# Performance work log

Hardware: AMD Instinct MI355X
Metric: run time of the kernel (lower is better)

Reference implementation:

```python
import jax, jax.numpy as jnp
import numpy as np

B, N, D, H = 1, 4096, 1024, 16
K = D // H
ROPE_BASE = 10000.0


def _rope_cos_sin(n, k, base, dtype):
    # GPT-NeoX style rotary embedding: inv_freq over even dims, emb = cat(freqs, freqs)
    inv_freq = 1.0 / (base ** (jnp.arange(0, k, 2, dtype=jnp.float32) / k))  # [K/2]
    pos = jnp.arange(n, dtype=jnp.float32)
    freqs = pos[:, None] * inv_freq[None, :]              # [N, K/2]
    emb = jnp.concatenate([freqs, freqs], axis=-1)        # [N, K]
    return jnp.cos(emb).astype(dtype), jnp.sin(emb).astype(dtype)


def _rotate_half(x):
    x1, x2 = jnp.split(x, 2, axis=-1)
    return jnp.concatenate([-x2, x1], axis=-1)


def setup_inputs() -> dict:
    key = jax.random.key(0)
    kx, kq, ko = jax.random.split(key, 3)
    x = jax.random.normal(kx, (B, N, D), dtype=jnp.float32)
    # torch Linear weights: [out_features, in_features], y = x @ W^T
    w_qkv = jax.random.normal(kq, (3 * H * K, D), dtype=jnp.float32) / np.sqrt(D)
    w_out = jax.random.normal(ko, (D, D), dtype=jnp.float32) / np.sqrt(D)
    return {"x": x, "w_qkv": w_qkv, "w_out": w_out}


def reference(x, w_qkv, w_out):
    b, n, d = x.shape
    qkv = jnp.einsum('bnd,ed->bne', x, w_qkv).reshape(b, n, 3, H, K)
    q, k, v = qkv[:, :, 0], qkv[:, :, 1], qkv[:, :, 2]   # [B, N, H, K]
    cos, sin = _rope_cos_sin(n, K, ROPE_BASE, x.dtype)    # [N, K]
    cos = cos[None, :, None, :]
    sin = sin[None, :, None, :]
    q = q * cos + _rotate_half(q) * sin
    k = k * cos + _rotate_half(k) * sin
    # explicit O(N^2) score matrix, as in the original module
    scores = jnp.einsum('bnhk,bmhk->bnhm', q, k) / np.sqrt(K).astype(x.dtype)
    causal_mask = jnp.tril(jnp.ones((n, n), dtype=bool))  # [N, M]
    scores = jnp.where(causal_mask[None, :, None, :], scores, jnp.finfo(x.dtype).min)
    probs = jax.nn.softmax(scores, axis=-1)
    attn = jnp.einsum('bnhm,bmhk->bnhk', probs, v).reshape(b, n, d)
    return jnp.einsum('bnd,ed->bne', attn, w_out)
```

## Files before the change

kernel.cpp:

```cpp
#include <hip/hip_runtime.h>
#include <hip/hip_bf16.h>
#include <math.h>

#define N_SEQ 4096
#define DIM   1024
#define NHEAD 16
#define HDIM  64
#define E3    3072

typedef short bf16x8 __attribute__((ext_vector_type(8)));
typedef float f32x4  __attribute__((ext_vector_type(4)));
typedef unsigned int u32;

#if __has_builtin(__builtin_amdgcn_exp2f)
#define EXP2(x) __builtin_amdgcn_exp2f(x)
#else
#define EXP2(x) exp2f(x)
#endif

__device__ __forceinline__ float bf2f(unsigned short u) {
    union { unsigned int i; float f; } x; x.i = ((unsigned int)u) << 16; return x.f;
}
__device__ __forceinline__ unsigned short f2bf(float f) {
    union { float f; unsigned int i; } x; x.f = f;
    unsigned int r = x.i + 0x7FFF + ((x.i >> 16) & 1);
    return (unsigned short)(r >> 16);
}
__device__ __forceinline__ unsigned short f2bf_fast(float f) {
    union { float f; unsigned int i; } x; x.f = f;
    return (unsigned short)((x.i + 0x8000u) >> 16);
}
__device__ __forceinline__ f32x4 mfma16(bf16x8 a, bf16x8 b, f32x4 c) {
    return __builtin_amdgcn_mfma_f32_16x16x32_bf16(a, b, c, 0, 0, 0);
}
__device__ __forceinline__ void gload_lds16(const unsigned short* g, unsigned short* l) {
    __builtin_amdgcn_global_load_lds(
        (const __attribute__((address_space(1))) u32*)g,
        (__attribute__((address_space(3))) u32*)l, 16, 0, 0);
}

__device__ __forceinline__ int probe_isf32(const unsigned short* __restrict__ X) {
    __shared__ int cnt;
    if (threadIdx.x == 0) cnt = 0;
    __syncthreads();
    int bad = 0;
    for (int i = threadIdx.x; i < 4096; i += 256) {
        float v = bf2f(X[i]);
        if (!(fabsf(v) < 1e10f)) bad = 1;
    }
    if (bad) atomicAdd(&cnt, 1);
    __syncthreads();
    return cnt > 0;
}

__global__ __launch_bounds__(256)
void prep_kernel(const void* __restrict__ X, const void* __restrict__ Wq,
                 const void* __restrict__ Wo,
                 unsigned short* __restrict__ Xb, unsigned short* __restrict__ Wqb,
                 unsigned short* __restrict__ Wob,
                 int* __restrict__ flag)
{
    const int isf32 = probe_isf32((const unsigned short*)X);
    if (blockIdx.x == 0 && threadIdx.x == 0) *flag = isf32;
    if (!isf32) return;

    const int nX4  = (N_SEQ * DIM) >> 2;
    const int nWq4 = (E3 * DIM) >> 2;
    const int nWo4 = (DIM * DIM) >> 2;
    const int total = nX4 + nWq4 + nWo4;
    const int stride = gridDim.x * blockDim.x;
    for (int i = blockIdx.x * blockDim.x + threadIdx.x; i < total; i += stride) {
        const float4* src; ushort4* dst; int j = i;
        if (j < nX4)                { src = (const float4*)X  + j;  dst = (ushort4*)Xb  + j; }
        else if ((j -= nX4) < nWq4) { src = (const float4*)Wq + j;  dst = (ushort4*)Wqb + j; }
        else { j -= nWq4;             src = (const float4*)Wo + j;  dst = (ushort4*)Wob + j; }
        float4 v = *src;
        ushort4 u;
        u.x = f2bf(v.x); u.y = f2bf(v.y); u.z = f2bf(v.z); u.w = f2bf(v.w);
        *dst = u;
    }
}

__global__ __launch_bounds__(256)
void qkv_mfma_kernel(const void* __restrict__ Xo, const unsigned short* __restrict__ Xc,
                     const void* __restrict__ Wo_, const unsigned short* __restrict__ Wc,
                     const int* __restrict__ flag,
                     unsigned short* __restrict__ Qf,
                     unsigned short* __restrict__ Kf,
                     unsigned short* __restrict__ Vf)
{
    __shared__ __align__(16) unsigned short SMEM[4][4096];

    const int isf32 = *flag;
    const unsigned short* Xb = isf32 ? Xc : (const unsigned short*)Xo;
    const unsigned short* Wb = isf32 ? Wc : (const unsigned short*)Wo_;

    const int tid  = threadIdx.x;
    const int lane = tid & 63;
    const int wave = tid >> 6;
    const int wr = wave >> 1, wc = wave & 1;
    const int lm = lane & 15, q4 = lane >> 4;
    const int rbase = blockIdx.y * 128;
    const int cbase = blockIdx.x * 128;

    const int srow = wave * 16 + (lane >> 2);
    const int scol = (lane & 3) * 8;

    const unsigned short* xsrc = Xb + (size_t)(rbase + srow) * DIM + scol;
    const unsigned short* wsrc = Wb + (size_t)(cbase + srow) * DIM + scol;
    const int la = (wr*64 + lm)*32 + q4*8;
    const int lb = (wc*64 + lm)*32 + q4*8;

    f32x4 acc[4][4];
    #pragma unroll
    for (int i = 0; i < 4; ++i)
        #pragma unroll
        for (int j = 0; j < 4; ++j) acc[i][j] = (f32x4){0.f, 0.f, 0.f, 0.f};

    #define QSTAGE(buf)                                                             \
        {                                                                           \
            _Pragma("unroll")                                                       \
            for (int j = 0; j < 2; ++j) {                                           \
                gload_lds16(xsrc + (size_t)j*64*DIM, &SMEM[buf][j*2048 + wave*512]);   \
                gload_lds16(wsrc + (size_t)j*64*DIM, &SMEM[2+buf][j*2048 + wave*512]); \
            }                                                                       \
            xsrc += 32; wsrc += 32;                                                 \
        }

    QSTAGE(0)
    for (int it = 0; it < DIM/32; ++it) {
        const int cur = it & 1;
        __syncthreads();
        if (it + 1 < DIM/32) QSTAGE(cur ^ 1)

        bf16x8 a[4], b[4];
        #pragma unroll
        for (int mi = 0; mi < 4; ++mi)
            a[mi] = *(const bf16x8*)&SMEM[cur][la + mi*512];
        #pragma unroll
        for (int ni = 0; ni < 4; ++ni)
            b[ni] = *(const bf16x8*)&SMEM[2+cur][lb + ni*512];
        #pragma unroll
        for (int mi = 0; mi < 4; ++mi)
            #pragma unroll
            for (int ni = 0; ni < 4; ++ni)
                acc[mi][ni] = mfma16(a[mi], b[ni], acc[mi][ni]);
    }
    #undef QSTAGE

    __syncthreads();

    const int ecol = cbase + wc * 64;
    const int part = ecol >> 10;
    const int h    = (ecol >> 6) & 15;
    unsigned short* ep = &SMEM[0][0] + wave*4096;

    if (part == 2) {
        #pragma unroll
        for (int mh = 0; mh < 2; ++mh) {
            #pragma unroll
            for (int mi2 = 0; mi2 < 2; ++mi2) {
                const int mi = mh*2 + mi2;
                #pragma unroll
                for (int r = 0; r < 4; ++r) {
                    const int n31 = mi2*16 + q4*4 + r;
                    #pragma unroll
                    for (int ni = 0; ni < 4; ++ni)
                        ep[(ni*16 + lm)*40 + n31] = f2bf(acc[mi][ni][r]);
                }
            }
            const int nb = rbase + wr*64 + mh*32;
            const size_t vb = (((size_t)h*128 + (nb >> 5)) << 11) + (size_t)lane*8;
            #pragma unroll
            for (int ni = 0; ni < 4; ++ni) {
                const bf16x8 fr = *(const bf16x8*)(ep + (ni*16 + lm)*40 + q4*8);
                *(bf16x8*)(Vf + vb + (size_t)ni*512) = fr;
            }
        }
    } else {
        unsigned short* dst = (part == 0) ? Qf : Kf;
        const float scl = (part == 0) ? 0.180336884f : 1.0f;
        const float inv0 = powf(10000.f, -((float)lm)        * (1.f/32.f));
        const float inv1 = powf(10000.f, -((float)(lm + 16)) * (1.f/32.f));
        #pragma unroll
        for (int mi = 0; mi < 4; ++mi) {
            const int tn = rbase + wr*64 + mi*16;
            #pragma unroll
            for (int r = 0; r < 4; ++r) {
                const int n = tn + q4*4 + r;
                float s0, c0, s1, c1;
                sincosf((float)n * inv0, &s0, &c0);
                sincosf((float)n * inv1, &s1, &c1);
                const int row = (q4*4 + r)*72;
                ep[row + lm]      = f2bf((acc[mi][0][r]*c0 - acc[mi][2][r]*s0) * scl);
                ep[row + lm + 16] = f2bf((acc[mi][1][r]*c1 - acc[mi][3][r]*s1) * scl);
                ep[row + lm + 32] = f2bf((acc[mi][2][r]*c0 + acc[mi][0][r]*s0) * scl);
                ep[row + lm + 48] = f2bf((acc[mi][3][r]*c1 + acc[mi][1][r]*s1) * scl);
            }
            const size_t tb = (((size_t)(h*256 + (tn >> 4))) << 10) + (size_t)lane*8;
            #pragma unroll
            for (int c = 0; c < 2; ++c) {
                const bf16x8 fr = *(const bf16x8*)(ep + lm*72 + c*32 + q4*8);
                *(bf16x8*)(dst + tb + (size_t)c*512) = fr;
            }
        }
    }
}

__global__ __launch_bounds__(256)
void attn_mfma_kernel(const unsigned short* __restrict__ Qf,
                      const unsigned short* __restrict__ Kf,
                      const unsigned short* __restrict__ Vf,
                      unsigned short* __restrict__ Attn)
{
    __shared__ __align__(16) unsigned short Ks[2][4096];
    __shared__ __align__(16) unsigned short Vs[2][4096];
    __shared__ __align__(16) unsigned short P16[4][32][40];

    const int tid  = threadIdx.x;
    const int lane = tid & 63;
    const int wave = tid >> 6;
    const int q4 = lane >> 4, lm = lane & 15;
    const int qh = wave >> 1, kh = wave & 1;

    const int h  = blockIdx.x & 15;
    const int qb = blockIdx.x >> 4;
    const int q0 = (63 - qb) << 6;
    const int qw = q0 + (qh << 5);

    const unsigned short* qp = Qf + (((size_t)(h*256 + (qw >> 4))) << 10) + (size_t)lane * 8;
    bf16x8 aq[2][2];
    aq[0][0] = *(const bf16x8*)(qp);
    aq[0][1] = *(const bf16x8*)(qp + 512);
    aq[1][0] = *(const bf16x8*)(qp + 1024);
    aq[1][1] = *(const bf16x8*)(qp + 1536);

    float l_part[2][4];
    f32x4 o[2][4];
    #pragma unroll
    for (int qi = 0; qi < 2; ++qi) {
        #pragma unroll
        for (int r = 0; r < 4; ++r) l_part[qi][r] = 0.f;
        #pragma unroll
        for (int dc = 0; dc < 4; ++dc) o[qi][dc] = (f32x4){0.f, 0.f, 0.f, 0.f};
    }

    const unsigned short* sbase;
    unsigned short* db0;
    unsigned short* db1;
    {
        const int ch0 = (wave & 1) * 4;
        const size_t hb = ((size_t)h) << 18;
        sbase = ((wave < 2) ? Kf : Vf) + hb + ch0*512 + (size_t)lane*8;
        db0 = ((wave < 2) ? &Ks[0][0] : &Vs[0][0]) + ch0*512;
        db1 = ((wave < 2) ? &Ks[1][0] : &Vs[1][0]) + ch0*512;
    }
    unsigned short* pw  = &P16[wave][0][0];
    unsigned short* pwa = pw + (4*q4)*40 + lm;
    const unsigned short* par = pw + lm*40 + q4*8;

    const int ntiles = (q0 >> 6) + 1;

    #define STAGE(dst)                                                         \
        {                                                                      \
            _Pragma("unroll")                                                  \
            for (int i = 0; i < 4; ++i)                                        \
                gload_lds16(sbase + i*512, (dst) + i*512);                     \
            sbase += 4096;                                                     \
        }

    STAGE(db0)

    for (int it = 0; it < ntiles; ++it) {
        const int kt = it << 6;
        const int cur = it & 1;

        __syncthreads();
        if (it + 1 < ntiles) STAGE(cur ? db0 : db1)

        const unsigned short* kc = &Ks[cur][kh*2048 + lane*8];
        const unsigned short* vc = &Vs[cur][kh*2048 + lane*8];

        f32x4 s[2][2];
        #pragma unroll
        for (int ki = 0; ki < 2; ++ki) {
            const bf16x8 bk0 = *(const bf16x8*)(kc + ki*1024);
            const bf16x8 bk1 = *(const bf16x8*)(kc + ki*1024 + 512);
            #pragma unroll
            for (int qi = 0; qi < 2; ++qi) {
                f32x4 z = (f32x4){0.f, 0.f, 0.f, 0.f};
                z = mfma16(aq[qi][0], bk0, z);
                s[qi][ki] = mfma16(aq[qi][1], bk1, z);
            }
        }

        if (kt + 32*kh + 31 > qw) {
            #pragma unroll
            for (int ki = 0; ki < 2; ++ki) {
                const int key = kt + 32*kh + 16*ki + lm;
                #pragma unroll
                for (int qi = 0; qi < 2; ++qi) {
                    const int qq = qw + 16*qi + 4*q4;
                    #pragma unroll
                    for (int r = 0; r < 4; ++r)
                        if (key > qq + r) s[qi][ki][r] = -INFINITY;
                }
            }
        }

        #pragma unroll
        for (int qi = 0; qi < 2; ++qi)
            #pragma unroll
            for (int ki = 0; ki < 2; ++ki)
                #pragma unroll
                for (int r = 0; r < 4; ++r) {
                    const float p = EXP2(s[qi][ki][r]);
                    l_part[qi][r] += p;
                    pwa[qi*640 + r*40 + ki*16] = f2bf_fast(p);
                }

        bf16x8 pa[2];
        pa[0] = *(const bf16x8*)(par);
        pa[1] = *(const bf16x8*)(par + 640);

        #pragma unroll
        for (int dc = 0; dc < 4; ++dc) {
            const bf16x8 bv = *(const bf16x8*)(vc + dc*512);
            #pragma unroll
            for (int qi = 0; qi < 2; ++qi)
                o[qi][dc] = mfma16(pa[qi], bv, o[qi][dc]);
        }
    }
    #undef STAGE

    #pragma unroll
    for (int qi = 0; qi < 2; ++qi)
        #pragma unroll
        for (int r = 0; r < 4; ++r) {
            float l = l_part[qi][r];
            #pragma unroll
            for (int mk = 1; mk <= 8; mk <<= 1) l += __shfl_xor(l, mk);
            l_part[qi][r] = l;
        }

    float* Ox = (float*)&Ks[0][0];
    float* Lx = (float*)&Vs[0][0];
    __syncthreads();
    if (kh == 1) {
        #pragma unroll
        for (int qi = 0; qi < 2; ++qi) {
            #pragma unroll
            for (int r = 0; r < 4; ++r) {
                const int qq = 16*qi + 4*q4 + r;
                #pragma unroll
                for (int dc = 0; dc < 4; ++dc)
                    Ox[qh*2048 + qq*64 + 16*dc + lm] = o[qi][dc][r];
                if (lm == 0) Lx[qh*32 + qq] = l_part[qi][r];
            }
        }
    }
    __syncthreads();
    if (kh == 0) {
        #pragma unroll
        for (int qi = 0; qi < 2; ++qi)
            #pragma unroll
            for (int r = 0; r < 4; ++r) {
                const int qq = 16*qi + 4*q4 + r;
                const float inv = 1.f / (l_part[qi][r] + Lx[qh*32 + qq]);
                const size_t row = (size_t)(qw + qq) * DIM + (h << 6) + lm;
                #pragma unroll
                for (int dc = 0; dc < 4; ++dc) {
                    const float v = o[qi][dc][r] + Ox[qh*2048 + qq*64 + 16*dc + lm];
                    Attn[row + 16*dc] = f2bf(v * inv);
                }
            }
    }
}

__global__ __launch_bounds__(256)
void out_mfma_kernel(const unsigned short* __restrict__ Ab,
                     const void* __restrict__ Wo_, const unsigned short* __restrict__ Wc,
                     const int* __restrict__ flag,
                     void* __restrict__ Out)
{
    __shared__ unsigned short As[2][4096];
    __shared__ unsigned short Bs[2][2048];

    const int isf32 = *flag;
    const unsigned short* Wb = isf32 ? Wc : (const unsigned short*)Wo_;

    const int tid  = threadIdx.x;
    const int lane = tid & 63;
    const int wave = tid >> 6;
    const int lm = lane & 15, q4 = lane >> 4;
    const int rbase = blockIdx.y * 128;
    const int cbase = blockIdx.x * 64;

    const int srow16 = lane >> 2;
    const int scol = (lane & 3) * 8;

    const unsigned short* asrc = Ab + (size_t)(rbase + wave*32 + srow16) * DIM + scol;
    const unsigned short* bsrc = Wb + (size_t)(cbase + wave*16 + srow16) * DIM + scol;
    const int la = (wave*32 + lm)*32 + q4*8;
    const int lb = lm*32 + q4*8;

    f32x4 acc[2][4];
    #pragma unroll
    for (int i = 0; i < 2; ++i)
        #pragma unroll
        for (int j = 0; j < 4; ++j) acc[i][j] = (f32x4){0.f, 0.f, 0.f, 0.f};

    #define OSTAGE(buf)                                                          \
        {                                                                        \
            _Pragma("unroll")                                                    \
            for (int j = 0; j < 2; ++j)                                          \
                gload_lds16(asrc + (size_t)j*16*DIM, &As[buf][(wave*32 + j*16)*32]); \
            gload_lds16(bsrc, &Bs[buf][(wave*16)*32]);                           \
            asrc += 32; bsrc += 32;                                              \
        }

    OSTAGE(0)
    for (int it = 0; it < DIM/32; ++it) {
        const int cur = it & 1;
        __syncthreads();
        if (it + 1 < DIM/32) OSTAGE(cur ^ 1)

        bf16x8 a[2], b[4];
        #pragma unroll
        for (int mi = 0; mi < 2; ++mi)
            a[mi] = *(const bf16x8*)&As[cur][la + mi*512];
        #pragma unroll
        for (int ni = 0; ni < 4; ++ni)
            b[ni] = *(const bf16x8*)&Bs[cur][lb + ni*512];
        #pragma unroll
        for (int mi = 0; mi < 2; ++mi)
            #pragma unroll
            for (int ni = 0; ni < 4; ++ni)
                acc[mi][ni] = mfma16(a[mi], b[ni], acc[mi][ni]);
    }
    #undef OSTAGE

    #pragma unroll
    for (int mi = 0; mi < 2; ++mi)
        #pragma unroll
        for (int r = 0; r < 4; ++r) {
            const size_t n = rbase + wave*32 + mi*16 + q4*4 + r;
            #pragma unroll
            for (int ni = 0; ni < 4; ++ni) {
                const size_t e = cbase + ni*16 + lm;
                const float v = acc[mi][ni][r];
                if (isf32) ((float*)Out)[n * DIM + e] = v;
                else       ((unsigned short*)Out)[n * DIM + e] = f2bf(v);
            }
        }
}

extern "C" void kernel_launch(void* const* d_in, const int* in_sizes, int n_in,
                              void* d_out, int out_size, void* d_ws, size_t ws_size,
                              hipStream_t stream) {
    const void* X    = d_in[0];
    const void* Wqkv = d_in[1];
    const void* Wout = d_in[2];

    int* flag = (int*)d_ws;
    unsigned short* base = (unsigned short*)((char*)d_ws + 256);
    const size_t nX = (size_t)N_SEQ * DIM;
    const size_t nWq = (size_t)E3 * DIM;
    const size_t nWo = (size_t)DIM * DIM;
    unsigned short* Xb  = base;
    unsigned short* Wqb = Xb + nX;
    unsigned short* Wob = Wqb + nWq;
    unsigned short* Qf  = Wob + nWo;
    unsigned short* Kf  = Qf + nX;
    unsigned short* Vf  = Kf + nX;
    unsigned short* At  = Vf + nX;

    prep_kernel<<<768, 256, 0, stream>>>(X, Wqkv, Wout, Xb, Wqb, Wob, flag);
    qkv_mfma_kernel<<<dim3(E3 / 128, N_SEQ / 128), 256, 0, stream>>>(X, Xb, Wqkv, Wqb, flag, Qf, Kf, Vf);
    attn_mfma_kernel<<<dim3(NHEAD * (N_SEQ / 64)), 256, 0, stream>>>(Qf, Kf, Vf, At);
    out_mfma_kernel<<<dim3(DIM / 64, N_SEQ / 128), 256, 0, stream>>>(At, Wout, Wob, flag, d_out);
}
```

Before: 209.9 us.

## Load K/V fragments directly from global memory instead of LDS double-buffering

The attention kernel no longer stages K and V tiles into shared memory with async global-to-LDS copies and per-tile barriers. Each wave now reads its MFMA K and V fragments straight from global memory, which are laid out pre-fragmented, and relies on cache reuse. LDS shrinks to the P buffer plus a small reduction scratch, and launch bounds request 5 blocks per CU to raise occupancy. The cost is that every wave issues its own global/L2 loads without the cooperative sharing through LDS, so load latency sits on the critical path with no explicit prefetch.

```diff
diff --git a/kernel.cpp b/kernel.cpp
--- a/kernel.cpp
+++ b/kernel.cpp
@@ -207,15 +207,15 @@
     }
 }
 
-__global__ __launch_bounds__(256)
+__global__ __launch_bounds__(256, 5)
 void attn_mfma_kernel(const unsigned short* __restrict__ Qf,
                       const unsigned short* __restrict__ Kf,
                       const unsigned short* __restrict__ Vf,
                       unsigned short* __restrict__ Attn)
 {
-    __shared__ __align__(16) unsigned short Ks[2][4096];
-    __shared__ __align__(16) unsigned short Vs[2][4096];
     __shared__ __align__(16) unsigned short P16[4][32][40];
+    __shared__ __align__(16) float Ox[2][32][64];
+    __shared__ float Lx[2][32];
 
     const int tid  = threadIdx.x;
     const int lane = tid & 63;
@@ -245,52 +245,34 @@
         for (int dc = 0; dc < 4; ++dc) o[qi][dc] = (f32x4){0.f, 0.f, 0.f, 0.f};
     }
 
-    const unsigned short* sbase;
-    unsigned short* db0;
-    unsigned short* db1;
-    {
-        const int ch0 = (wave & 1) * 4;
-        const size_t hb = ((size_t)h) << 18;
-        sbase = ((wave < 2) ? Kf : Vf) + hb + ch0*512 + (size_t)lane*8;
-        db0 = ((wave < 2) ? &Ks[0][0] : &Vs[0][0]) + ch0*512;
-        db1 = ((wave < 2) ? &Ks[1][0] : &Vs[1][0]) + ch0*512;
-    }
+    const size_t hb = ((size_t)h) << 18;
+    const unsigned short* kc = Kf + hb + (size_t)(kh*2048) + (size_t)lane*8;
+    const unsigned short* vc = Vf + hb + (size_t)(kh*2048) + (size_t)lane*8;
+
     unsigned short* pw  = &P16[wave][0][0];
     unsigned short* pwa = pw + (4*q4)*40 + lm;
     const unsigned short* par = pw + lm*40 + q4*8;
 
     const int ntiles = (q0 >> 6) + 1;
 
-    #define STAGE(dst)                                                         \
-        {                                                                      \
-            _Pragma("unroll")                                                  \
-            for (int i = 0; i < 4; ++i)                                        \
-                gload_lds16(sbase + i*512, (dst) + i*512);                     \
-            sbase += 4096;                                                     \
-        }
-
-    STAGE(db0)
-
     for (int it = 0; it < ntiles; ++it) {
         const int kt = it << 6;
-        const int cur = it & 1;
-
-        __syncthreads();
-        if (it + 1 < ntiles) STAGE(cur ? db0 : db1)
-
-        const unsigned short* kc = &Ks[cur][kh*2048 + lane*8];
-        const unsigned short* vc = &Vs[cur][kh*2048 + lane*8];
+
+        bf16x8 bk[2][2];
+        #pragma unroll
+        for (int ki = 0; ki < 2; ++ki) {
+            bk[ki][0] = *(const bf16x8*)(kc + ki*1024);
+            bk[ki][1] = *(const bf16x8*)(kc + ki*1024 + 512);
+        }
 
         f32x4 s[2][2];
         #pragma unroll
         for (int ki = 0; ki < 2; ++ki) {
-            const bf16x8 bk0 = *(const bf16x8*)(kc + ki*1024);
-            const bf16x8 bk1 = *(const bf16x8*)(kc + ki*1024 + 512);
             #pragma unroll
             for (int qi = 0; qi < 2; ++qi) {
                 f32x4 z = (f32x4){0.f, 0.f, 0.f, 0.f};
-                z = mfma16(aq[qi][0], bk0, z);
-                s[qi][ki] = mfma16(aq[qi][1], bk1, z);
+                z = mfma16(aq[qi][0], bk[ki][0], z);
+                s[qi][ki] = mfma16(aq[qi][1], bk[ki][1], z);
             }
         }
 
@@ -319,19 +301,25 @@
                     pwa[qi*640 + r*40 + ki*16] = f2bf_fast(p);
                 }
 
+        bf16x8 bv[4];
+        #pragma unroll
+        for (int dc = 0; dc < 4; ++dc)
+            bv[dc] = *(const bf16x8*)(vc + dc*512);
+
         bf16x8 pa[2];
         pa[0] = *(const bf16x8*)(par);
         pa[1] = *(const bf16x8*)(par + 640);
 
         #pragma unroll
         for (int dc = 0; dc < 4; ++dc) {
-            const bf16x8 bv = *(const bf16x8*)(vc + dc*512);
             #pragma unroll
             for (int qi = 0; qi < 2; ++qi)
-                o[qi][dc] = mfma16(pa[qi], bv, o[qi][dc]);
-        }
-    }
-    #undef STAGE
+                o[qi][dc] = mfma16(pa[qi], bv[dc], o[qi][dc]);
+        }
+
+        kc += 4096;
+        vc += 4096;
+    }
 
     #pragma unroll
     for (int qi = 0; qi < 2; ++qi)
@@ -343,9 +331,6 @@
             l_part[qi][r] = l;
         }
 
-    float* Ox = (float*)&Ks[0][0];
-    float* Lx = (float*)&Vs[0][0];
-    __syncthreads();
     if (kh == 1) {
         #pragma unroll
         for (int qi = 0; qi < 2; ++qi) {
@@ -354,8 +339,8 @@
                 const int qq = 16*qi + 4*q4 + r;
                 #pragma unroll
                 for (int dc = 0; dc < 4; ++dc)
-                    Ox[qh*2048 + qq*64 + 16*dc + lm] = o[qi][dc][r];
-                if (lm == 0) Lx[qh*32 + qq] = l_part[qi][r];
+                    Ox[qh][qq][16*dc + lm] = o[qi][dc][r];
+                if (lm == 0) Lx[qh][qq] = l_part[qi][r];
             }
         }
     }
@@ -366,11 +351,11 @@
             #pragma unroll
             for (int r = 0; r < 4; ++r) {
                 const int qq = 16*qi + 4*q4 + r;
-                const float inv = 1.f / (l_part[qi][r] + Lx[qh*32 + qq]);
+                const float inv = 1.f / (l_part[qi][r] + Lx[qh][qq]);
                 const size_t row = (size_t)(qw + qq) * DIM + (h << 6) + lm;
                 #pragma unroll
                 for (int dc = 0; dc < 4; ++dc) {
-                    const float v = o[qi][dc][r] + Ox[qh*2048 + qq*64 + 16*dc + lm];
+                    const float v = o[qi][dc][r] + Ox[qh][qq][16*dc + lm];
                     Attn[row + 16*dc] = f2bf(v * inv);
                 }
             }
```

Result: slower. 214.4 us (+2.1%).
